# Optimization experiments

Hardware: AMD Instinct MI355X
Metric: run time of the kernel (lower is better)

The kernel has to match this reference:

```python
import jax, jax.numpy as jnp
import numpy as np


def polymatmul(x, d):
    """Matrix multiply of 2x2 matrices whose entries are polynomials.

    x: (b, n, 2, 2, d1)  -- batch of per-diagonal-block 2x2 polynomial matrices
    d: (n, 2, 2, d2)     -- per-block 2x2 polynomial matrices (the diagonal params)
    Returns: (b, n, 2, 2, d1 + d2 - 1)
    out[b,n,i,j,:] = sum_k full_conv(x[b,n,i,k,:], d[n,k,j,:])
    Implemented by looping over the (small) d2 coefficient axis and accumulating
    shifted 2x2 matmuls, so the only large intermediate is the output itself.
    """
    d1 = x.shape[-1]
    d2 = d.shape[-1]
    out = jnp.zeros(x.shape[:-1] + (d1 + d2 - 1,), dtype=x.dtype)
    for v in range(d2):
        # contract over k (the inner 2-dim), broadcast over poly coeff axis u
        term = jnp.einsum('bniku,nkj->bniju', x, d[..., v])
        out = out.at[..., v:v + d1].add(term)
    return out


def setup_inputs() -> dict:
    key = jax.random.key(0)
    k1, k2, k3 = jax.random.split(key, 3)
    size, deg = 8192, 7
    b, d1 = 64, 16
    input_ = jax.random.normal(k1, (b, 2 * size, 2, 2, d1), dtype=jnp.float32)
    diag1 = jax.random.normal(k2, (size, 2, 2, deg + 1), dtype=jnp.float32)
    diag2 = jax.random.normal(k3, (size, 2, 2, deg + 1), dtype=jnp.float32)
    return {"input_": input_, "diag1": diag1, "diag2": diag2}


def reference(input_, diag1, diag2):
    size = diag1.shape[0]
    # HstackDiag.forward: sum of the two polynomial block-diagonal matmuls
    return polymatmul(input_[:, :size], diag1) + polymatmul(input_[:, size:], diag2)
```

## Files before the change

### kernel.cpp

```cpp
#include <hip/hip_runtime.h>

#define BB 64
#define NN 8192
#define TILE 64
#define DOUT 23

__device__ __forceinline__ void compute_half(const float4* __restrict__ sbuf,
                                             const float4* __restrict__ dp,
                                             int unit, int i, float acc[DOUT]) {
#pragma unroll
    for (int k = 0; k < 2; ++k) {
        float4 dq0 = dp[k * 4 + 0];
        float4 dq1 = dp[k * 4 + 1];
        const float dv[8] = {dq0.x, dq0.y, dq0.z, dq0.w,
                             dq1.x, dq1.y, dq1.z, dq1.w};
#pragma unroll
        for (int q = 0; q < 4; ++q) {
            const int G = unit * 16 + i * 8 + k * 4 + q;
            float4 xq = sbuf[G ^ ((G >> 3) & 7)];
            const float xe[4] = {xq.x, xq.y, xq.z, xq.w};
#pragma unroll
            for (int e = 0; e < 4; ++e) {
#pragma unroll
                for (int v = 0; v < 8; ++v) {
                    acc[q * 4 + e + v] += xe[e] * dv[v];
                }
            }
        }
    }
}

__global__ __launch_bounds__(256) void hstackdiag_kernel(
    const float* __restrict__ input,
    const float* __restrict__ diag1,
    const float* __restrict__ diag2,
    float* __restrict__ out) {
    __shared__ float4 sbuf[1024];

    const int t = threadIdx.x;
    const int bx = blockIdx.x;
    const int b = bx >> 7;
    const int n0 = (bx & 127) * TILE;

    const float4* g1 = (const float4*)input + ((size_t)b * (2 * NN) + n0) * 16;
    const float4* g2 = g1 + (size_t)NN * 16;

    const int j = t & 1;
    const int i = (t >> 1) & 1;
    const int unit = t >> 2;
    const int n = n0 + unit;
    const float4* dp1 = (const float4*)diag1 + (size_t)n * 8 + j * 2;
    const float4* dp2 = (const float4*)diag2 + (size_t)n * 8 + j * 2;

    float acc[DOUT];
#pragma unroll
    for (int u = 0; u < DOUT; ++u) acc[u] = 0.0f;

    {
        float4 r[4];
#pragma unroll
        for (int rr = 0; rr < 4; ++rr) r[rr] = g1[rr * 256 + t];
#pragma unroll
        for (int rr = 0; rr < 4; ++rr) {
            const int G = rr * 256 + t;
            sbuf[G ^ ((G >> 3) & 7)] = r[rr];
        }
    }
    __syncthreads();

    compute_half(sbuf, dp1, unit, i, acc);

    __syncthreads();

    {
        float4 r[4];
#pragma unroll
        for (int rr = 0; rr < 4; ++rr) r[rr] = g2[rr * 256 + t];
#pragma unroll
        for (int rr = 0; rr < 4; ++rr) {
            const int G = rr * 256 + t;
            sbuf[G ^ ((G >> 3) & 7)] = r[rr];
        }
    }
    __syncthreads();

    compute_half(sbuf, dp2, unit, i, acc);

    __syncthreads();

    float* sout = (float*)sbuf;
    const int c = i * 2 + j;
    float* gout = out + ((size_t)b * NN + n0) * (4 * DOUT);

#pragma unroll
    for (int p = 0; p < 2; ++p) {
        if ((unit >> 5) == p) {
#pragma unroll
            for (int q = 0; q < DOUT; ++q)
                sout[(unit & 31) * 92 + c * DOUT + q] = acc[q];
        }
        __syncthreads();
#pragma unroll
        for (int rr = 0; rr < 11; ++rr)
            gout[p * 2944 + rr * 256 + t] = sout[rr * 256 + t];
        if (t < 128) gout[p * 2944 + 2816 + t] = sout[2816 + t];
        if (p == 0) __syncthreads();
    }
}

extern "C" void kernel_launch(void* const* d_in, const int* in_sizes, int n_in,
                              void* d_out, int out_size, void* d_ws, size_t ws_size,
                              hipStream_t stream) {
    const float* input = (const float*)d_in[0];
    const float* diag1 = (const float*)d_in[1];
    const float* diag2 = (const float*)d_in[2];
    float* out = (float*)d_out;

    const int grid = BB * (NN / TILE);
    hstackdiag_kernel<<<grid, 256, 0, stream>>>(input, diag1, diag2, out);
}
```

Measured before the change: 88.08 us.

## Split output coefficients across two thread halves with smaller tile

Halves the tile to 32 blocks per workgroup and gives each output element to two threads: one accumulates coefficients 0-11 and the other 12-22. Register pressure per thread drops from 23 accumulators to 12, which may raise occupancy, and the grid doubles. Both input halves are now loaded into registers up front, so the second global load overlaps the first compute phase. The cost is duplicated reads of the diagonal parameters and some x values, plus more workgroups that each do less work.

```diff
diff --git a/kernel.cpp b/kernel.cpp
--- a/kernel.cpp
+++ b/kernel.cpp
@@ -2,28 +2,53 @@
 
 #define BB 64
 #define NN 8192
-#define TILE 64
+#define TILE 32
 #define DOUT 23
 
-__device__ __forceinline__ void compute_half(const float4* __restrict__ sbuf,
-                                             const float4* __restrict__ dp,
-                                             int unit, int i, float acc[DOUT]) {
+__device__ __forceinline__ int swz(int G) { return G ^ ((G >> 3) & 7); }
+
+__device__ __forceinline__ void compute_low(const float4* __restrict__ sbuf,
+                                            const float4* __restrict__ dp,
+                                            int unit, int i, float* __restrict__ acc) {
 #pragma unroll
     for (int k = 0; k < 2; ++k) {
-        float4 dq0 = dp[k * 4 + 0];
-        float4 dq1 = dp[k * 4 + 1];
+        float4 dq0 = dp[k * 4 + 0], dq1 = dp[k * 4 + 1];
         const float dv[8] = {dq0.x, dq0.y, dq0.z, dq0.w,
                              dq1.x, dq1.y, dq1.z, dq1.w};
 #pragma unroll
-        for (int q = 0; q < 4; ++q) {
-            const int G = unit * 16 + i * 8 + k * 4 + q;
-            float4 xq = sbuf[G ^ ((G >> 3) & 7)];
+        for (int q = 0; q < 3; ++q) {
+            float4 xq = sbuf[swz(unit * 16 + i * 8 + k * 4 + q)];
             const float xe[4] = {xq.x, xq.y, xq.z, xq.w};
 #pragma unroll
             for (int e = 0; e < 4; ++e) {
+                const int u = q * 4 + e;
 #pragma unroll
                 for (int v = 0; v < 8; ++v) {
-                    acc[q * 4 + e + v] += xe[e] * dv[v];
+                    if (u + v < 12) acc[u + v] += xe[e] * dv[v];
+                }
+            }
+        }
+    }
+}
+
+__device__ __forceinline__ void compute_high(const float4* __restrict__ sbuf,
+                                             const float4* __restrict__ dp,
+                                             int unit, int i, float* __restrict__ acc) {
+#pragma unroll
+    for (int k = 0; k < 2; ++k) {
+        float4 dq0 = dp[k * 4 + 0], dq1 = dp[k * 4 + 1];
+        const float dv[8] = {dq0.x, dq0.y, dq0.z, dq0.w,
+                             dq1.x, dq1.y, dq1.z, dq1.w};
+#pragma unroll
+        for (int q = 1; q < 4; ++q) {
+            float4 xq = sbuf[swz(unit * 16 + i * 8 + k * 4 + q)];
+            const float xe[4] = {xq.x, xq.y, xq.z, xq.w};
+#pragma unroll
+            for (int e = 0; e < 4; ++e) {
+                const int u = q * 4 + e;
+#pragma unroll
+                for (int v = 0; v < 8; ++v) {
+                    if (u + v >= 12) acc[u + v - 12] += xe[e] * dv[v];
                 }
             }
         }
@@ -35,57 +60,42 @@
     const float* __restrict__ diag1,
     const float* __restrict__ diag2,
     float* __restrict__ out) {
-    __shared__ float4 sbuf[1024];
+    __shared__ float4 sbuf[512];
 
     const int t = threadIdx.x;
     const int bx = blockIdx.x;
-    const int b = bx >> 7;
-    const int n0 = (bx & 127) * TILE;
+    const int b = bx >> 8;
+    const int n0 = (bx & 255) * TILE;
 
     const float4* g1 = (const float4*)input + ((size_t)b * (2 * NN) + n0) * 16;
     const float4* g2 = g1 + (size_t)NN * 16;
 
     const int j = t & 1;
     const int i = (t >> 1) & 1;
-    const int unit = t >> 2;
+    const int unit = (t >> 2) & 31;
+    const int wh = t >> 7;
     const int n = n0 + unit;
     const float4* dp1 = (const float4*)diag1 + (size_t)n * 8 + j * 2;
     const float4* dp2 = (const float4*)diag2 + (size_t)n * 8 + j * 2;
 
-    float acc[DOUT];
-#pragma unroll
-    for (int u = 0; u < DOUT; ++u) acc[u] = 0.0f;
-
-    {
-        float4 r[4];
-#pragma unroll
-        for (int rr = 0; rr < 4; ++rr) r[rr] = g1[rr * 256 + t];
-#pragma unroll
-        for (int rr = 0; rr < 4; ++rr) {
-            const int G = rr * 256 + t;
-            sbuf[G ^ ((G >> 3) & 7)] = r[rr];
-        }
-    }
+    float4 s0 = g1[t], s1 = g1[256 + t];
+    float4 p0 = g2[t], p1 = g2[256 + t];
+    sbuf[swz(t)] = s0;
+    sbuf[swz(256 + t)] = s1;
     __syncthreads();
 
-    compute_half(sbuf, dp1, unit, i, acc);
+    float acc[12];
+#pragma unroll
+    for (int u = 0; u < 12; ++u) acc[u] = 0.0f;
 
+    if (wh == 0) compute_low(sbuf, dp1, unit, i, acc);
+    else         compute_high(sbuf, dp1, unit, i, acc);
     __syncthreads();
-
-    {
-        float4 r[4];
-#pragma unroll
-        for (int rr = 0; rr < 4; ++rr) r[rr] = g2[rr * 256 + t];
-#pragma unroll
-        for (int rr = 0; rr < 4; ++rr) {
-            const int G = rr * 256 + t;
-            sbuf[G ^ ((G >> 3) & 7)] = r[rr];
-        }
-    }
+    sbuf[swz(t)] = p0;
+    sbuf[swz(256 + t)] = p1;
     __syncthreads();
-
-    compute_half(sbuf, dp2, unit, i, acc);
-
+    if (wh == 0) compute_low(sbuf, dp2, unit, i, acc);
+    else         compute_high(sbuf, dp2, unit, i, acc);
     __syncthreads();
 
     float* sout = (float*)sbuf;
@@ -94,16 +104,21 @@
 
 #pragma unroll
     for (int p = 0; p < 2; ++p) {
-        if ((unit >> 5) == p) {
+        if ((unit >> 4) == p) {
+            const int base = (unit & 15) * 92 + c * DOUT;
+            if (wh == 0) {
 #pragma unroll
-            for (int q = 0; q < DOUT; ++q)
-                sout[(unit & 31) * 92 + c * DOUT + q] = acc[q];
+                for (int q = 0; q < 12; ++q) sout[base + q] = acc[q];
+            } else {
+#pragma unroll
+                for (int q = 0; q < 11; ++q) sout[base + 12 + q] = acc[q];
+            }
         }
         __syncthreads();
 #pragma unroll
-        for (int rr = 0; rr < 11; ++rr)
-            gout[p * 2944 + rr * 256 + t] = sout[rr * 256 + t];
-        if (t < 128) gout[p * 2944 + 2816 + t] = sout[2816 + t];
+        for (int rr = 0; rr < 5; ++rr)
+            gout[p * 1472 + rr * 256 + t] = sout[rr * 256 + t];
+        if (t < 192) gout[p * 1472 + 1280 + t] = sout[1280 + t];
         if (p == 0) __syncthreads();
     }
 }
```

After: 93.03 us. 5.6% more time.

## Process four tiles per block with register-prefetched input and float4 output stores

Applied to the files above, without the earlier changes.

Each block now loops over four consecutive tiles instead of handling one. The next half-tile's input is prefetched into registers while the current half is computed from shared memory, which is meant to overlap global loads with compute. Output copy-out switches from scalar float stores to float4 stores. The grid shrinks by a factor of four, which reduces the number of waves and the block launch overhead but lowers parallelism and adds register pressure.

```diff
diff --git a/kernel.cpp b/kernel.cpp
--- a/kernel.cpp
+++ b/kernel.cpp
@@ -4,20 +4,21 @@
 #define NN 8192
 #define TILE 64
 #define DOUT 23
+#define TPB 4
+
+__device__ __forceinline__ int swz(int G) { return G ^ ((G >> 3) & 7); }
 
 __device__ __forceinline__ void compute_half(const float4* __restrict__ sbuf,
                                              const float4* __restrict__ dp,
-                                             int unit, int i, float acc[DOUT]) {
+                                             int unit, int i, float* __restrict__ acc) {
 #pragma unroll
     for (int k = 0; k < 2; ++k) {
-        float4 dq0 = dp[k * 4 + 0];
-        float4 dq1 = dp[k * 4 + 1];
+        float4 dq0 = dp[k * 4 + 0], dq1 = dp[k * 4 + 1];
         const float dv[8] = {dq0.x, dq0.y, dq0.z, dq0.w,
                              dq1.x, dq1.y, dq1.z, dq1.w};
 #pragma unroll
         for (int q = 0; q < 4; ++q) {
-            const int G = unit * 16 + i * 8 + k * 4 + q;
-            float4 xq = sbuf[G ^ ((G >> 3) & 7)];
+            float4 xq = sbuf[swz(unit * 16 + i * 8 + k * 4 + q)];
             const float xe[4] = {xq.x, xq.y, xq.z, xq.w};
 #pragma unroll
             for (int e = 0; e < 4; ++e) {
@@ -38,73 +39,74 @@
     __shared__ float4 sbuf[1024];
 
     const int t = threadIdx.x;
-    const int bx = blockIdx.x;
-    const int b = bx >> 7;
-    const int n0 = (bx & 127) * TILE;
-
-    const float4* g1 = (const float4*)input + ((size_t)b * (2 * NN) + n0) * 16;
-    const float4* g2 = g1 + (size_t)NN * 16;
-
+    const int tile0 = blockIdx.x * TPB;
+    const int b = tile0 >> 7;
     const int j = t & 1;
     const int i = (t >> 1) & 1;
     const int unit = t >> 2;
-    const int n = n0 + unit;
-    const float4* dp1 = (const float4*)diag1 + (size_t)n * 8 + j * 2;
-    const float4* dp2 = (const float4*)diag2 + (size_t)n * 8 + j * 2;
 
-    float acc[DOUT];
+    const float4* gbase = (const float4*)input + (size_t)b * (2 * NN) * 16;
+    int n0 = (tile0 & 127) * TILE;
+
+    float4 R[4];
+    {
+        const float4* g1 = gbase + (size_t)n0 * 16;
 #pragma unroll
-    for (int u = 0; u < DOUT; ++u) acc[u] = 0.0f;
+        for (int r = 0; r < 4; ++r) R[r] = g1[r * 256 + t];
+    }
 
-    {
-        float4 r[4];
-#pragma unroll
-        for (int rr = 0; rr < 4; ++rr) r[rr] = g1[rr * 256 + t];
-#pragma unroll
-        for (int rr = 0; rr < 4; ++rr) {
-            const int G = rr * 256 + t;
-            sbuf[G ^ ((G >> 3) & 7)] = r[rr];
-        }
-    }
-    __syncthreads();
+    for (int tt = 0; tt < TPB; ++tt) {
+        const int n = n0 + unit;
+        const float4* dp1 = (const float4*)diag1 + (size_t)n * 8 + j * 2;
+        const float4* dp2 = (const float4*)diag2 + (size_t)n * 8 + j * 2;
 
-    compute_half(sbuf, dp1, unit, i, acc);
-
-    __syncthreads();
-
-    {
-        float4 r[4];
-#pragma unroll
-        for (int rr = 0; rr < 4; ++rr) r[rr] = g2[rr * 256 + t];
-#pragma unroll
-        for (int rr = 0; rr < 4; ++rr) {
-            const int G = rr * 256 + t;
-            sbuf[G ^ ((G >> 3) & 7)] = r[rr];
-        }
-    }
-    __syncthreads();
-
-    compute_half(sbuf, dp2, unit, i, acc);
-
-    __syncthreads();
-
-    float* sout = (float*)sbuf;
-    const int c = i * 2 + j;
-    float* gout = out + ((size_t)b * NN + n0) * (4 * DOUT);
-
-#pragma unroll
-    for (int p = 0; p < 2; ++p) {
-        if ((unit >> 5) == p) {
-#pragma unroll
-            for (int q = 0; q < DOUT; ++q)
-                sout[(unit & 31) * 92 + c * DOUT + q] = acc[q];
-        }
         __syncthreads();
 #pragma unroll
-        for (int rr = 0; rr < 11; ++rr)
-            gout[p * 2944 + rr * 256 + t] = sout[rr * 256 + t];
-        if (t < 128) gout[p * 2944 + 2816 + t] = sout[2816 + t];
-        if (p == 0) __syncthreads();
+        for (int r = 0; r < 4; ++r) sbuf[swz(r * 256 + t)] = R[r];
+        __syncthreads();
+        {
+            const float4* g2 = gbase + (size_t)(NN + n0) * 16;
+#pragma unroll
+            for (int r = 0; r < 4; ++r) R[r] = g2[r * 256 + t];
+        }
+
+        float acc[DOUT];
+#pragma unroll
+        for (int u = 0; u < DOUT; ++u) acc[u] = 0.0f;
+        compute_half(sbuf, dp1, unit, i, acc);
+
+        __syncthreads();
+#pragma unroll
+        for (int r = 0; r < 4; ++r) sbuf[swz(r * 256 + t)] = R[r];
+        __syncthreads();
+        if (tt < TPB - 1) {
+            const float4* g1n = gbase + (size_t)(n0 + TILE) * 16;
+#pragma unroll
+            for (int r = 0; r < 4; ++r) R[r] = g1n[r * 256 + t];
+        }
+        compute_half(sbuf, dp2, unit, i, acc);
+
+        __syncthreads();
+
+        float* sout = (float*)sbuf;
+        float4* sout4 = sbuf;
+        float* gout = out + ((size_t)b * NN + n0) * (4 * DOUT);
+        const int c = i * 2 + j;
+#pragma unroll
+        for (int p = 0; p < 2; ++p) {
+            if ((unit >> 5) == p) {
+#pragma unroll
+                for (int q = 0; q < DOUT; ++q)
+                    sout[(unit & 31) * 92 + c * DOUT + q] = acc[q];
+            }
+            __syncthreads();
+            float4* g4 = (float4*)(gout + p * 2944);
+#pragma unroll
+            for (int rr = 0; rr < 2; ++rr) g4[rr * 256 + t] = sout4[rr * 256 + t];
+            if (t < 224) g4[512 + t] = sout4[512 + t];
+            if (p == 0) __syncthreads();
+        }
+        n0 += TILE;
     }
 }
 
@@ -116,6 +118,6 @@
     const float* diag2 = (const float*)d_in[2];
     float* out = (float*)d_out;
 
-    const int grid = BB * (NN / TILE);
+    const int grid = BB * (NN / TILE) / TPB;
     hstackdiag_kernel<<<grid, 256, 0, stream>>>(input, diag1, diag2, out);
 }
```

After: 145.7 us. 65.4% more time.
